# Kernel tuning notes

Hardware: AMD Instinct MI355X
Metric: run time of the kernel (lower is better)

Reference implementation:

```python
import jax, jax.numpy as jnp
import numpy as np


def setup_inputs() -> dict:
    key = jax.random.key(0)
    k1, k2 = jax.random.split(key)
    pred_m = jax.random.normal(k1, (64, 1, 512, 512), dtype=jnp.float32)
    # boxes: (x, y, s_x, s_y) per (batch, frame, target); values in [0, 256)
    multi_targets = jax.random.randint(k2, (64, 5, 32, 4), 0, 256, dtype=jnp.int32)
    return {"pred_m": pred_m, "multi_targets": multi_targets}


def _paint_heatmap(multi_targets, B, H, W, dtype):
    """Vectorized replacement for the triple-nested box-fill loop.

    Uses a 2D difference-array scatter + double cumsum: each box adds
    +1/-1 at its four corners; after prefix sums, count>0 marks painted
    pixels (original sets them to 255 regardless of overlap).
    """
    gt = multi_targets.reshape(B, -1, 4)  # [B, N, 4], N = n_frames*n_targets
    x, y, sx, sy = gt[..., 0], gt[..., 1], gt[..., 2], gt[..., 3]
    # python slicing clamps the end of the slice at H/W
    x1 = jnp.minimum(x, H)
    y1 = jnp.minimum(y, W)
    x2 = jnp.minimum(x + sx, H)
    y2 = jnp.minimum(y + sy, W)
    b_idx = jnp.broadcast_to(jnp.arange(B)[:, None], x.shape)
    diff = jnp.zeros((B, H + 1, W + 1), jnp.int32)
    diff = diff.at[b_idx, x1, y1].add(1)
    diff = diff.at[b_idx, x1, y2].add(-1)
    diff = diff.at[b_idx, x2, y1].add(-1)
    diff = diff.at[b_idx, x2, y2].add(1)
    count = jnp.cumsum(jnp.cumsum(diff, axis=1), axis=2)[:, :H, :W]
    return (count > 0).astype(dtype) * jnp.asarray(255.0, dtype)


def reference(pred_m, multi_targets):
    B, _, H, W = pred_m.shape
    heatmap = _paint_heatmap(multi_targets, B, H, W, pred_m.dtype)  # [B, H, W]
    target = heatmap[:, None]            # [B, 1, H, W]
    pred = jax.nn.sigmoid(pred_m)        # [B, 1, H, W]
    smooth = jnp.asarray(1.0, pred_m.dtype)
    intersection = jnp.sum(pred * target, axis=(1, 2, 3))
    pred_sum = jnp.sum(pred, axis=(1, 2, 3))
    target_sum = jnp.sum(target, axis=(1, 2, 3))
    loss = (intersection + smooth) / (pred_sum + target_sum - intersection + smooth)
    return 1.0 - jnp.mean(loss)
```

## Files before the change

### kernel.cpp

```cpp
#include <hip/hip_runtime.h>
#include <math.h>

#define SLICES 32
#define ROWS_PER_SLICE 16
#define NBOXES 160

static __device__ __forceinline__ float fast_sigmoid(float x) {
    return __builtin_amdgcn_rcpf(1.0f + __expf(-x));
}

__global__ __launch_bounds__(256) void mask_kernel(
    const int* __restrict__ targets, unsigned* __restrict__ gmask)
{
    const int t = threadIdx.x;
    const int slice = blockIdx.x;
    const int b = blockIdx.y;
    const int r0 = slice * ROWS_PER_SLICE;
    const int lane = t & 63;

    const int4* tg = (const int4*)targets + (size_t)b * NBOXES;
    int4 gb0 = tg[lane];
    int4 gb1 = tg[64 + lane];
    int4 gb2 = (lane < 32) ? tg[128 + lane] : make_int4(0, 0, 0, 0);

    unsigned px0, py0, px1, py1, px2, py2;
    auto clip = [&](int4 g, unsigned& px, unsigned& py) -> bool {
        int x1 = min(g.x, 512), y1 = min(g.y, 512);
        int x2 = min(g.x + g.z, 512), y2 = min(g.y + g.w, 512);
        int cx1 = max(x1, r0), cx2 = min(x2, r0 + ROWS_PER_SLICE);
        px = (unsigned)cx1 | ((unsigned)cx2 << 16);
        py = (unsigned)y1 | ((unsigned)y2 << 16);
        return (cx2 > cx1) && (y2 > y1);
    };
    bool k0 = clip(gb0, px0, py0);
    bool k1 = clip(gb1, px1, py1);
    bool k2 = clip(gb2, px2, py2) && (lane < 32);
    unsigned long long m0 = __ballot(k0);
    unsigned long long m1 = __ballot(k1);
    unsigned long long m2 = __ballot(k2);

    const int r = r0 + (t >> 4);
    const unsigned wb = (unsigned)(t & 15) * 32u;
    unsigned m = 0;
    auto scan = [&](unsigned long long mk, unsigned px, unsigned py) {
        while (mk) {
            int k = (int)__builtin_ctzll(mk);
            mk &= mk - 1;
            unsigned rx = (unsigned)__builtin_amdgcn_readlane((int)px, k);
            unsigned ry = (unsigned)__builtin_amdgcn_readlane((int)py, k);
            int x1 = (int)(rx & 0xffffu), x2 = (int)(rx >> 16);
            unsigned y1 = ry & 0xffffu, y2 = ry >> 16;
            bool in_row = (r >= x1) && (r < x2);
            unsigned lo = y1 > wb ? y1 : wb;
            unsigned hi = y2 < wb + 32u ? y2 : wb + 32u;
            int nn = (int)hi - (int)lo;
            unsigned bits = 0xFFFFFFFFu >> ((32 - nn) & 31);
            unsigned contrib = bits << ((lo - wb) & 31u);
            m |= (in_row && nn > 0) ? contrib : 0u;
        }
    };
    scan(m0, px0, py0);
    scan(m1, px1, py1);
    scan(m2, px2, py2);
    gmask[(size_t)b * 8192 + (size_t)r0 * 16 + t] = m;
}

__global__ __launch_bounds__(256, 6) void stream_kernel(
    const float* __restrict__ pred, const unsigned* __restrict__ gmask,
    float* __restrict__ partials)
{
    const int t = threadIdx.x;
    const int slice = blockIdx.x;
    const int b = blockIdx.y;
    const int r0 = slice * ROWS_PER_SLICE;
    const int lane = t & 63, wave = t >> 6;
    const int col4 = t & 127;
    const int rb = t >> 7;
    const int widx = col4 >> 3;
    const unsigned bb = (unsigned)(col4 & 7) * 4u;

    const unsigned* gm = gmask + (size_t)b * 8192 + (size_t)(r0 + rb) * 16 + widx;
    unsigned w0 = gm[0 * 32];
    unsigned w1 = gm[1 * 32];
    unsigned w2 = gm[2 * 32];
    unsigned w3 = gm[3 * 32];
    unsigned w4 = gm[4 * 32];
    unsigned w5 = gm[5 * 32];
    unsigned w6 = gm[6 * 32];
    unsigned w7 = gm[7 * 32];

    const float4* p4 = (const float4*)pred;
    const size_t g0 = (size_t)b * 65536 + (size_t)(r0 + rb) * 128 + col4;
    float4 v0 = p4[g0 + 0 * 256];
    float4 v1 = p4[g0 + 1 * 256];
    float4 v2 = p4[g0 + 2 * 256];
    float4 v3 = p4[g0 + 3 * 256];
    float4 v4 = p4[g0 + 4 * 256];
    float4 v5 = p4[g0 + 5 * 256];
    float4 v6 = p4[g0 + 6 * 256];
    float4 v7 = p4[g0 + 7 * 256];

    float psum = 0.0f, isum = 0.0f;
    int cnt = 0;
#define ACC(V, W)                                                       \
    {                                                                   \
        const unsigned n = ((W) >> bb) & 0xFu;                          \
        float s0 = fast_sigmoid((V).x);                                 \
        float s1 = fast_sigmoid((V).y);                                 \
        float s2 = fast_sigmoid((V).z);                                 \
        float s3 = fast_sigmoid((V).w);                                 \
        psum += (s0 + s1) + (s2 + s3);                                  \
        cnt += __popc(n);                                               \
        isum += ((n & 1u) ? s0 : 0.0f) + ((n & 2u) ? s1 : 0.0f)         \
              + ((n & 4u) ? s2 : 0.0f) + ((n & 8u) ? s3 : 0.0f);        \
    }
    ACC(v0, w0) ACC(v1, w1) ACC(v2, w2) ACC(v3, w3)
    ACC(v4, w4) ACC(v5, w5) ACC(v6, w6) ACC(v7, w7)
#undef ACC
    float csum = (float)cnt;

    for (int off = 32; off > 0; off >>= 1) {
        psum += __shfl_down(psum, off);
        isum += __shfl_down(isum, off);
        csum += __shfl_down(csum, off);
    }
    if (lane == 0) {
        float* o = partials + (((size_t)b * SLICES + slice) * 4 + wave) * 3;
        o[0] = psum; o[1] = isum; o[2] = csum;
    }
}

__global__ __launch_bounds__(64) void final_kernel(
    const float* __restrict__ partials, float* __restrict__ out)
{
    const int b = threadIdx.x;
    double P = 0, I = 0, C = 0;
    const float* p = partials + (size_t)b * SLICES * 4 * 3;
    for (int s = 0; s < SLICES * 4; ++s) {
        P += (double)p[s * 3 + 0];
        I += (double)p[s * 3 + 1];
        C += (double)p[s * 3 + 2];
    }
    const double inter = 255.0 * I;
    const double tsum  = 255.0 * C;
    double loss = (inter + 1.0) / (P + tsum - inter + 1.0);
    for (int off = 32; off > 0; off >>= 1) loss += __shfl_down(loss, off);
    if (b == 0) out[0] = (float)(1.0 - loss / 64.0);
}

extern "C" void kernel_launch(void* const* d_in, const int* in_sizes, int n_in,
                              void* d_out, int out_size, void* d_ws, size_t ws_size,
                              hipStream_t stream) {
    const float* pred    = (const float*)d_in[0];
    const int*   targets = (const int*)d_in[1];
    float* out = (float*)d_out;

    float* partials = (float*)d_ws;
    unsigned* gmask = (unsigned*)((char*)d_ws + (96 << 10));

    dim3 grid(SLICES, 64);
    mask_kernel<<<grid, 256, 0, stream>>>(targets, gmask);
    stream_kernel<<<grid, 256, 0, stream>>>(pred, gmask, partials);
    final_kernel<<<1, 64, 0, stream>>>(partials, out);
}
```

Baseline: 118.7 us.

## Fuse mask painting into the sigmoid reduction kernel

Merges the box-mask kernel into the streaming reduction kernel. Each thread now builds the 4-bit masks for its own 8 rows directly from the ballot-compacted box list, so the global bitmask buffer and one kernel launch are gone. The pred loads are issued before the box scan so their latency can overlap it. In exchange, each thread does roughly eight times more compare work per box inside the scan loop and holds more live registers.

```diff
diff --git a/kernel.cpp b/kernel.cpp
--- a/kernel.cpp
+++ b/kernel.cpp
@@ -4,24 +4,40 @@
 #define SLICES 32
 #define ROWS_PER_SLICE 16
 #define NBOXES 160
+#define THREADS 256
 
 static __device__ __forceinline__ float fast_sigmoid(float x) {
     return __builtin_amdgcn_rcpf(1.0f + __expf(-x));
 }
 
-__global__ __launch_bounds__(256) void mask_kernel(
-    const int* __restrict__ targets, unsigned* __restrict__ gmask)
+__global__ __launch_bounds__(THREADS, 6) void paint_reduce_kernel(
+    const float* __restrict__ pred, const int* __restrict__ targets,
+    float* __restrict__ partials)
 {
     const int t = threadIdx.x;
     const int slice = blockIdx.x;
     const int b = blockIdx.y;
     const int r0 = slice * ROWS_PER_SLICE;
-    const int lane = t & 63;
+    const int lane = t & 63, wave = t >> 6;
+    const int col4 = t & 127;
+    const int rb = t >> 7;
+    const int c0 = col4 * 4;
 
     const int4* tg = (const int4*)targets + (size_t)b * NBOXES;
     int4 gb0 = tg[lane];
     int4 gb1 = tg[64 + lane];
     int4 gb2 = (lane < 32) ? tg[128 + lane] : make_int4(0, 0, 0, 0);
+
+    const float4* p4 = (const float4*)pred;
+    const size_t g0 = (size_t)b * 65536 + (size_t)(r0 + rb) * 128 + col4;
+    float4 v0 = p4[g0 + 0 * 256];
+    float4 v1 = p4[g0 + 1 * 256];
+    float4 v2 = p4[g0 + 2 * 256];
+    float4 v3 = p4[g0 + 3 * 256];
+    float4 v4 = p4[g0 + 4 * 256];
+    float4 v5 = p4[g0 + 5 * 256];
+    float4 v6 = p4[g0 + 6 * 256];
+    float4 v7 = p4[g0 + 7 * 256];
 
     unsigned px0, py0, px1, py1, px2, py2;
     auto clip = [&](int4 g, unsigned& px, unsigned& py) -> bool {
@@ -35,87 +51,48 @@
     bool k0 = clip(gb0, px0, py0);
     bool k1 = clip(gb1, px1, py1);
     bool k2 = clip(gb2, px2, py2) && (lane < 32);
-    unsigned long long m0 = __ballot(k0);
-    unsigned long long m1 = __ballot(k1);
-    unsigned long long m2 = __ballot(k2);
+    unsigned long long bm0 = __ballot(k0);
+    unsigned long long bm1 = __ballot(k1);
+    unsigned long long bm2 = __ballot(k2);
 
-    const int r = r0 + (t >> 4);
-    const unsigned wb = (unsigned)(t & 15) * 32u;
-    unsigned m = 0;
+    unsigned m[8] = {0, 0, 0, 0, 0, 0, 0, 0};
     auto scan = [&](unsigned long long mk, unsigned px, unsigned py) {
         while (mk) {
             int k = (int)__builtin_ctzll(mk);
             mk &= mk - 1;
             unsigned rx = (unsigned)__builtin_amdgcn_readlane((int)px, k);
             unsigned ry = (unsigned)__builtin_amdgcn_readlane((int)py, k);
-            int x1 = (int)(rx & 0xffffu), x2 = (int)(rx >> 16);
-            unsigned y1 = ry & 0xffffu, y2 = ry >> 16;
-            bool in_row = (r >= x1) && (r < x2);
-            unsigned lo = y1 > wb ? y1 : wb;
-            unsigned hi = y2 < wb + 32u ? y2 : wb + 32u;
-            int nn = (int)hi - (int)lo;
-            unsigned bits = 0xFFFFFFFFu >> ((32 - nn) & 31);
-            unsigned contrib = bits << ((lo - wb) & 31u);
-            m |= (in_row && nn > 0) ? contrib : 0u;
+            const int x1 = (int)(rx & 0xffffu), x2 = (int)(rx >> 16);
+            const int y1 = (int)(ry & 0xffffu), y2 = (int)(ry >> 16);
+            int lo = max(y1, c0), hi = min(y2, c0 + 4);
+            int nn = hi - lo;
+            unsigned nibw = (nn > 0) ? (((1u << nn) - 1u) << (lo - c0)) : 0u;
+#pragma unroll
+            for (int kk = 0; kk < 8; ++kk) {
+                const int r = r0 + rb + 2 * kk;
+                m[kk] |= (r >= x1 && r < x2) ? nibw : 0u;
+            }
         }
     };
-    scan(m0, px0, py0);
-    scan(m1, px1, py1);
-    scan(m2, px2, py2);
-    gmask[(size_t)b * 8192 + (size_t)r0 * 16 + t] = m;
-}
-
-__global__ __launch_bounds__(256, 6) void stream_kernel(
-    const float* __restrict__ pred, const unsigned* __restrict__ gmask,
-    float* __restrict__ partials)
-{
-    const int t = threadIdx.x;
-    const int slice = blockIdx.x;
-    const int b = blockIdx.y;
-    const int r0 = slice * ROWS_PER_SLICE;
-    const int lane = t & 63, wave = t >> 6;
-    const int col4 = t & 127;
-    const int rb = t >> 7;
-    const int widx = col4 >> 3;
-    const unsigned bb = (unsigned)(col4 & 7) * 4u;
-
-    const unsigned* gm = gmask + (size_t)b * 8192 + (size_t)(r0 + rb) * 16 + widx;
-    unsigned w0 = gm[0 * 32];
-    unsigned w1 = gm[1 * 32];
-    unsigned w2 = gm[2 * 32];
-    unsigned w3 = gm[3 * 32];
-    unsigned w4 = gm[4 * 32];
-    unsigned w5 = gm[5 * 32];
-    unsigned w6 = gm[6 * 32];
-    unsigned w7 = gm[7 * 32];
-
-    const float4* p4 = (const float4*)pred;
-    const size_t g0 = (size_t)b * 65536 + (size_t)(r0 + rb) * 128 + col4;
-    float4 v0 = p4[g0 + 0 * 256];
-    float4 v1 = p4[g0 + 1 * 256];
-    float4 v2 = p4[g0 + 2 * 256];
-    float4 v3 = p4[g0 + 3 * 256];
-    float4 v4 = p4[g0 + 4 * 256];
-    float4 v5 = p4[g0 + 5 * 256];
-    float4 v6 = p4[g0 + 6 * 256];
-    float4 v7 = p4[g0 + 7 * 256];
+    scan(bm0, px0, py0);
+    scan(bm1, px1, py1);
+    scan(bm2, px2, py2);
 
     float psum = 0.0f, isum = 0.0f;
     int cnt = 0;
-#define ACC(V, W)                                                       \
+#define ACC(V, N)                                                       \
     {                                                                   \
-        const unsigned n = ((W) >> bb) & 0xFu;                          \
         float s0 = fast_sigmoid((V).x);                                 \
         float s1 = fast_sigmoid((V).y);                                 \
         float s2 = fast_sigmoid((V).z);                                 \
         float s3 = fast_sigmoid((V).w);                                 \
         psum += (s0 + s1) + (s2 + s3);                                  \
-        cnt += __popc(n);                                               \
-        isum += ((n & 1u) ? s0 : 0.0f) + ((n & 2u) ? s1 : 0.0f)         \
-              + ((n & 4u) ? s2 : 0.0f) + ((n & 8u) ? s3 : 0.0f);        \
+        cnt += __popc(N);                                               \
+        isum += (((N) & 1u) ? s0 : 0.0f) + (((N) & 2u) ? s1 : 0.0f)     \
+              + (((N) & 4u) ? s2 : 0.0f) + (((N) & 8u) ? s3 : 0.0f);    \
     }
-    ACC(v0, w0) ACC(v1, w1) ACC(v2, w2) ACC(v3, w3)
-    ACC(v4, w4) ACC(v5, w5) ACC(v6, w6) ACC(v7, w7)
+    ACC(v0, m[0]) ACC(v1, m[1]) ACC(v2, m[2]) ACC(v3, m[3])
+    ACC(v4, m[4]) ACC(v5, m[5]) ACC(v6, m[6]) ACC(v7, m[7])
 #undef ACC
     float csum = (float)cnt;
 
@@ -154,12 +131,9 @@
     const float* pred    = (const float*)d_in[0];
     const int*   targets = (const int*)d_in[1];
     float* out = (float*)d_out;
-
     float* partials = (float*)d_ws;
-    unsigned* gmask = (unsigned*)((char*)d_ws + (96 << 10));
 
     dim3 grid(SLICES, 64);
-    mask_kernel<<<grid, 256, 0, stream>>>(targets, gmask);
-    stream_kernel<<<grid, 256, 0, stream>>>(pred, gmask, partials);
+    paint_reduce_kernel<<<grid, THREADS, 0, stream>>>(pred, targets, partials);
     final_kernel<<<1, 64, 0, stream>>>(partials, out);
 }
```

Measured after the change: 148.3 us. +24.9%, slower.
